# Kernel optimization log

Measured on AMD Instinct MI355X. Metric: run time of the kernel, lower is better.

The kernel has to match this reference:

```python
import jax, jax.numpy as jnp
import numpy as np
from jax import lax

N_ITER = 50  # entmax-bisect iterations (entmax library default)
DEG = 12    # neighbors per node in global item graph


def entmax_bisect(X, alpha):
    # entmax with per-row alpha, over axis=1. X: [B, L, 1], alpha: [B, 1, 1]
    d = X.shape[1]
    Xa = X * (alpha - 1.0)
    inv = 1.0 / (alpha - 1.0)
    _p = lambda z: jnp.maximum(z, 0.0) ** inv
    max_val = jnp.max(Xa, axis=1, keepdims=True)
    tau_lo = max_val - 1.0                                   # _gp(1, alpha) = 1
    tau_hi = max_val - jnp.power(1.0 / d, alpha - 1.0)       # _gp(1/d, alpha)
    f_lo = jnp.sum(_p(Xa - tau_lo), axis=1, keepdims=True) - 1.0

    def body(i, carry):
        tau_lo, dm, _ = carry
        dm = dm * 0.5
        tau_m = tau_lo + dm
        f_m = jnp.sum(_p(Xa - tau_m), axis=1, keepdims=True) - 1.0
        tau_lo = jnp.where(f_m * f_lo >= 0.0, tau_m, tau_lo)
        return (tau_lo, dm, tau_m)

    tau_lo, dm, tau_m = lax.fori_loop(0, N_ITER, body, (tau_lo, tau_hi - tau_lo, tau_lo))
    p_m = _p(Xa - tau_m)
    return p_m / jnp.sum(p_m, axis=1, keepdims=True)  # ensure_sum_one


def setup_inputs() -> dict:
    key = jax.random.key(0)
    ks = jax.random.split(key, 10)
    B, L, D, N = 1024, 50, 256, 40000
    E = N * DEG
    stdv = 1.0 / np.sqrt(D)
    u = lambda k, shape: jax.random.uniform(k, shape, jnp.float32, -stdv, stdv)

    item_emb = u(ks[0], (N, D)).at[0].set(0.0)  # padding_idx=0
    items = jax.random.randint(ks[1], (B, L), 0, N)
    inputs_seq = jax.random.randint(ks[2], (B, L), 0, N)
    alias_inputs = jax.random.randint(ks[3], (B, L), 0, L)
    target_embedding = jax.random.normal(ks[4], (B, 1, 2 * D), jnp.float32)

    # sparse global item adjacency (row-normalized, DEG neighbors per node)
    adj_rows = jnp.repeat(jnp.arange(N, dtype=jnp.int32), DEG)
    adj_cols = jax.random.randint(ks[5], (E,), 0, N, dtype=jnp.int32)
    adj_vals = jax.random.uniform(ks[6], (E,), jnp.float32) / DEG

    kp = jax.random.split(ks[7], 10)
    return {
        "items": items, "inputs_seq": inputs_seq, "alias_inputs": alias_inputs,
        "target_embedding": target_embedding, "item_emb": item_emb,
        "adj_rows": adj_rows, "adj_cols": adj_cols, "adj_vals": adj_vals,
        "wf_w": u(kp[0], (D, 2 * D)), "wf_b": u(kp[1], (D,)),
        "alphaw_w": u(kp[2], (1, D)), "alphaw_b": u(kp[3], (1,)),
        "at_w0": u(kp[4], (1, D)), "at_w1": u(kp[5], (D, D)),
        "at_w2": u(kp[6], (D, D)), "at_bias": u(kp[7], (D,)),
    }


def reference(items, inputs_seq, alias_inputs, target_embedding, item_emb,
              adj_rows, adj_cols, adj_vals, wf_w, wf_b, alphaw_w, alphaw_b,
              at_w0, at_w1, at_w2, at_bias):
    N = item_emb.shape[0]
    # GlobalItemConv (1 layer): h = (x + adj @ x) / 2 via sparse SpMM
    agg = jax.ops.segment_sum(adj_vals[:, None] * item_emb[adj_cols], adj_rows,
                              num_segments=N)
    graph_embs = (item_emb + agg) * 0.5

    hidden = graph_embs[items]                              # [B, L, D] (dropout: eval)
    target_emb = target_embedding @ wf_w.T + wf_b           # [B, 1, D]

    # get_alpha: sigmoid + 1, then masked_fill(==1 -> 1.00001)
    alpha_ent = jax.nn.sigmoid(target_emb @ alphaw_w.T + alphaw_b) + 1.0  # [B,1,1]
    alpha_ent = jnp.where(alpha_ent == 1.0, 1.00001, alpha_ent)

    # tglobal_attention
    scores = jax.nn.relu(hidden @ at_w1 + target_emb @ at_w2 + at_bias) @ at_w0.T  # [B,L,1]
    attn = entmax_bisect(scores, alpha_ent)                 # sparse softmax over L
    c = jnp.einsum('blo,bld->bod', attn, hidden)[:, 0, :]   # alpha^T @ v, squeeze -> [B,D]

    c = jax.nn.selu(c)
    return c / jnp.linalg.norm(c, axis=-1, keepdims=True)
```

## Files before the change

kernel.cpp:

```cpp
#include <hip/hip_runtime.h>
#include <hip/hip_bf16.h>
#include <math.h>

#define BB 1024
#define LL 50
#define DD 256
#define TWO_D 512
#define NN 40000
#define DEG 12
#define NITER 50

typedef __attribute__((ext_vector_type(8))) short short8;
typedef __attribute__((ext_vector_type(4))) float floatx4;

__device__ __forceinline__ float wave_sum64(float v) {
#pragma unroll
    for (int off = 32; off > 0; off >>= 1) v += __shfl_xor(v, off, 64);
    return v;
}
__device__ __forceinline__ float wave_max64(float v) {
#pragma unroll
    for (int off = 32; off > 0; off >>= 1) v = fmaxf(v, __shfl_xor(v, off, 64));
    return v;
}
__device__ __forceinline__ float bf2f(ushort u) {
    union { unsigned int i; float f; } c; c.i = ((unsigned int)u) << 16; return c.f;
}
__device__ __forceinline__ ushort f2bf(float f) {
    __hip_bfloat16 h = __float2bfloat16(f);
    return *(ushort*)&h;
}
__device__ __forceinline__ float hw_exp2(float x) { return __builtin_amdgcn_exp2f(x); }
__device__ __forceinline__ float hw_log2(float x) { return __builtin_amdgcn_logf(x); }

__global__ __launch_bounds__(256) void k_emb_bf16(
    const float* __restrict__ emb, ushort* __restrict__ ebf)
{
    int i = (blockIdx.x * 256 + threadIdx.x) * 4;
    float4 v = *(const float4*)(emb + i);
    ushort4 o;
    o.x = f2bf(v.x); o.y = f2bf(v.y); o.z = f2bf(v.z); o.w = f2bf(v.w);
    *(ushort4*)(ebf + i) = o;
}

__global__ __launch_bounds__(256) void k_conv_all_bf16(
    const ushort* __restrict__ ebf, const int* __restrict__ adj_cols,
    const float* __restrict__ adj_vals, ushort* __restrict__ gbf)
{
    int wv = threadIdx.x >> 6, lane = threadIdx.x & 63;
    int n = blockIdx.x * 4 + wv;
    int colv = 0; float valv = 0.f;
    if (lane < DEG) { colv = adj_cols[n * DEG + lane]; valv = adj_vals[n * DEG + lane]; }
    ushort4 s = *(const ushort4*)(ebf + (size_t)n * DD + lane * 4);
    float a0 = bf2f(s.x), a1 = bf2f(s.y), a2 = bf2f(s.z), a3 = bf2f(s.w);
#pragma unroll
    for (int k = 0; k < DEG; ++k) {
        int   c = __shfl(colv, k, 64);
        float v = __shfl(valv, k, 64);
        ushort4 e = *(const ushort4*)(ebf + (size_t)c * DD + lane * 4);
        a0 += v * bf2f(e.x); a1 += v * bf2f(e.y);
        a2 += v * bf2f(e.z); a3 += v * bf2f(e.w);
    }
    ushort4 o;
    o.x = f2bf(0.5f * a0); o.y = f2bf(0.5f * a1);
    o.z = f2bf(0.5f * a2); o.w = f2bf(0.5f * a3);
    *(ushort4*)(gbf + (size_t)n * DD + lane * 4) = o;
}

__global__ __launch_bounds__(256) void k_conv_all_f32(
    const float* __restrict__ emb, const int* __restrict__ adj_cols,
    const float* __restrict__ adj_vals, ushort* __restrict__ gbf)
{
    int wv = threadIdx.x >> 6, lane = threadIdx.x & 63;
    int n = blockIdx.x * 4 + wv;
    int colv = 0; float valv = 0.f;
    if (lane < DEG) { colv = adj_cols[n * DEG + lane]; valv = adj_vals[n * DEG + lane]; }
    float4 s = *(const float4*)(emb + (size_t)n * DD + lane * 4);
    float a0 = s.x, a1 = s.y, a2 = s.z, a3 = s.w;
#pragma unroll
    for (int k = 0; k < DEG; ++k) {
        int   c = __shfl(colv, k, 64);
        float v = __shfl(valv, k, 64);
        float4 e = *(const float4*)(emb + (size_t)c * DD + lane * 4);
        a0 += v * e.x; a1 += v * e.y; a2 += v * e.z; a3 += v * e.w;
    }
    ushort4 o;
    o.x = f2bf(0.5f * a0); o.y = f2bf(0.5f * a1);
    o.z = f2bf(0.5f * a2); o.w = f2bf(0.5f * a3);
    *(ushort4*)(gbf + (size_t)n * DD + lane * 4) = o;
}

__global__ __launch_bounds__(256) void k_prep_w1(
    const float* __restrict__ at_w1, ushort* __restrict__ w1t)
{
    __shared__ ushort s[4][DD];
    int k0 = blockIdx.x * 4;
    int n = threadIdx.x;
#pragma unroll
    for (int j = 0; j < 4; ++j) s[j][n] = f2bf(at_w1[(k0 + j) * DD + n]);
    __syncthreads();
    ushort4 pk;
    pk.x = s[0][n]; pk.y = s[1][n]; pk.z = s[2][n]; pk.w = s[3][n];
    *(ushort4*)(w1t + n * DD + k0) = pk;
}

__global__ __launch_bounds__(256) void k_target(
    const float* __restrict__ tgt, const float* __restrict__ wf_w,
    const float* __restrict__ wf_b, float* __restrict__ te)
{
    const int BPB = 4;
    __shared__ float x_s[BPB * TWO_D];
    int b0 = blockIdx.x * BPB;
    int tid = threadIdx.x;
    for (int i = tid; i < BPB * TWO_D; i += 256) x_s[i] = tgt[b0 * TWO_D + i];
    __syncthreads();
    float bias = wf_b[tid];
    float acc[BPB];
#pragma unroll
    for (int j = 0; j < BPB; ++j) acc[j] = bias;
    const float4* w4 = (const float4*)(wf_w + tid * TWO_D);
    for (int kk = 0; kk < TWO_D / 4; ++kk) {
        float4 w = w4[kk];
#pragma unroll
        for (int j = 0; j < BPB; ++j) {
            const float* xs = x_s + j * TWO_D + kk * 4;
            acc[j] += xs[0] * w.x + xs[1] * w.y + xs[2] * w.z + xs[3] * w.w;
        }
    }
#pragma unroll
    for (int j = 0; j < BPB; ++j) te[(b0 + j) * DD + tid] = acc[j];
}

__global__ __launch_bounds__(256) void k_t2(
    const float* __restrict__ te, const float* __restrict__ at_w2,
    const float* __restrict__ at_bias, float* __restrict__ t2)
{
    const int BPB = 4;
    __shared__ float te_s[BPB * DD];
    int b0 = blockIdx.x * BPB;
    int tid = threadIdx.x;
    for (int i = tid; i < BPB * DD; i += 256) te_s[i] = te[b0 * DD + i];
    __syncthreads();
    float bias = at_bias[tid];
    float acc[BPB];
#pragma unroll
    for (int j = 0; j < BPB; ++j) acc[j] = bias;
    for (int k = 0; k < DD; ++k) {
        float w = at_w2[k * DD + tid];
#pragma unroll
        for (int j = 0; j < BPB; ++j) acc[j] += te_s[j * DD + k] * w;
    }
#pragma unroll
    for (int j = 0; j < BPB; ++j) t2[(b0 + j) * DD + tid] = acc[j];
}

__global__ __launch_bounds__(64) void k_alpha(
    const float* __restrict__ te, const float* __restrict__ aw,
    const float* __restrict__ ab, float* __restrict__ alpha)
{
    int b = blockIdx.x;
    int lane = threadIdx.x;
    float s = 0.f;
#pragma unroll
    for (int d = 0; d < DD; d += 64) s += te[b * DD + d + lane] * aw[d + lane];
    s = wave_sum64(s);
    if (lane == 0) {
        float x = s + ab[0];
        float sig = 1.f / (1.f + expf(-x));
        float a = 1.f + sig;
        if (a == 1.f) a = 1.00001f;
        alpha[b] = a;
    }
}

__global__ __launch_bounds__(256) void k_scores_mfma(
    const int* __restrict__ items, const ushort* __restrict__ gbf,
    const ushort* __restrict__ w1t, const float* __restrict__ t2,
    const float* __restrict__ at_w0, float* __restrict__ scores)
{
    __shared__ __align__(16) ushort sA[64 * 72];
    __shared__ __align__(16) ushort sB[256 * 72];
    __shared__ float sred[64][4];
    __shared__ int s_items[64];
    int tid = threadIdx.x;
    int blk = blockIdx.x;
    int lane = tid & 63, wv = tid >> 6;
    int cn = lane & 15, q = lane >> 4;
    int n0 = wv * 64;

    if (tid < 64) s_items[tid] = items[blk * 64 + tid];
    __syncthreads();

    floatx4 acc[4][4];
#pragma unroll
    for (int mt = 0; mt < 4; ++mt)
#pragma unroll
        for (int nt = 0; nt < 4; ++nt)
            acc[mt][nt] = (floatx4){0.f, 0.f, 0.f, 0.f};

#pragma unroll 1
    for (int kc = 0; kc < 4; ++kc) {
#pragma unroll
        for (int it = 0; it < 2; ++it) {
            int i = tid + it * 256;
            int row = i >> 3, seg = i & 7;
            *(uint4*)(sA + row * 72 + seg * 8) =
                *(const uint4*)(gbf + (size_t)s_items[row] * DD + kc * 64 + seg * 8);
        }
#pragma unroll
        for (int it = 0; it < 8; ++it) {
            int i = tid + it * 256;
            int n = i >> 3, seg = i & 7;
            *(uint4*)(sB + n * 72 + seg * 8) =
                *(const uint4*)(w1t + n * DD + kc * 64 + seg * 8);
        }
        __syncthreads();
#pragma unroll
        for (int ks = 0; ks < 2; ++ks) {
            short8 af[4], bfr[4];
#pragma unroll
            for (int mt = 0; mt < 4; ++mt)
                af[mt] = *(const short8*)(sA + (mt * 16 + cn) * 72 + ks * 32 + q * 8);
#pragma unroll
            for (int nt = 0; nt < 4; ++nt)
                bfr[nt] = *(const short8*)(sB + (n0 + nt * 16 + cn) * 72 + ks * 32 + q * 8);
#pragma unroll
            for (int mt = 0; mt < 4; ++mt)
#pragma unroll
                for (int nt = 0; nt < 4; ++nt)
                    acc[mt][nt] = __builtin_amdgcn_mfma_f32_16x16x32_bf16(
                        af[mt], bfr[nt], acc[mt][nt], 0, 0, 0);
        }
        __syncthreads();
    }

    float w0v[4];
#pragma unroll
    for (int nt = 0; nt < 4; ++nt) w0v[nt] = at_w0[n0 + nt * 16 + cn];
#pragma unroll
    for (int mt = 0; mt < 4; ++mt) {
#pragma unroll
        for (int r = 0; r < 4; ++r) {
            int row_in = q * 4 + r;
            int row_g = blk * 64 + mt * 16 + row_in;
            int b = row_g / LL;
            const float* t2b = t2 + b * DD;
            float p = 0.f;
#pragma unroll
            for (int nt = 0; nt < 4; ++nt) {
                int col = n0 + nt * 16 + cn;
                float v = acc[mt][nt][r] + t2b[col];
                p += fmaxf(v, 0.f) * w0v[nt];
            }
            p += __shfl_xor(p, 1, 64);
            p += __shfl_xor(p, 2, 64);
            p += __shfl_xor(p, 4, 64);
            p += __shfl_xor(p, 8, 64);
            if (cn == 0) sred[mt * 16 + row_in][wv] = p;
        }
    }
    __syncthreads();
    if (tid < 64)
        scores[blk * 64 + tid] = sred[tid][0] + sred[tid][1] + sred[tid][2] + sred[tid][3];
}

__device__ __forceinline__ float pw(float z, float invv) {
    return hw_exp2(invv * hw_log2(z));
}

__global__ __launch_bounds__(256) void k_entmax_out(
    const float* __restrict__ scores, const float* __restrict__ alpha,
    const int* __restrict__ items, const ushort* __restrict__ gbf,
    float* __restrict__ out)
{
    __shared__ float attn_s[LL];
    __shared__ int s_it[LL];
    __shared__ float red[4];
    int b = blockIdx.x;
    int tid = threadIdx.x;

    if (tid >= 192 && tid < 192 + LL) s_it[tid - 192] = items[b * LL + (tid - 192)];

    if (tid < 64) {
        int l = tid;
        float a = alpha[b];
        float am1 = a - 1.f;
        float invv = 1.f / am1;
        float x = (l < LL) ? scores[b * LL + l] : -__builtin_inff();
        float Xa = x * am1;

        float mx = wave_max64(Xa);
        float tau_lo = mx - 1.f;
        float tau_hi = mx - hw_exp2(am1 * hw_log2(1.f / (float)LL));

        float f_lo = wave_sum64(pw(fmaxf(Xa - tau_lo, 0.f), invv)) - 1.f;

        float dm = tau_hi - tau_lo;
        float tau_m = tau_lo;
#pragma unroll 1
        for (int it = 0; it < NITER; ++it) {
            dm *= 0.5f;
            tau_m = tau_lo + dm;
            float f_m = wave_sum64(pw(fmaxf(Xa - tau_m, 0.f), invv)) - 1.f;
            if (f_m * f_lo >= 0.f) tau_lo = tau_m;
        }
        float pm = pw(fmaxf(Xa - tau_m, 0.f), invv);
        float s = wave_sum64(pm);
        if (l < LL) attn_s[l] = pm / s;
    }
    __syncthreads();

    int d = tid;
    float c = 0.f;
#pragma unroll
    for (int l = 0; l < LL; ++l)
        c += attn_s[l] * bf2f(gbf[(size_t)s_it[l] * DD + d]);

    const float SC = 1.0507009873554805f;
    const float AL = 1.6732632423543772f;
    c = SC * (c > 0.f ? c : AL * expm1f(c));

    float ss = wave_sum64(c * c);
    int wv = tid >> 6, lane = tid & 63;
    if (lane == 0) red[wv] = ss;
    __syncthreads();
    float tot = red[0] + red[1] + red[2] + red[3];
    out[b * DD + d] = c / sqrtf(tot);
}

extern "C" void kernel_launch(void* const* d_in, const int* in_sizes, int n_in,
                              void* d_out, int out_size, void* d_ws, size_t ws_size,
                              hipStream_t stream) {
    const int*   items     = (const int*)  d_in[0];
    const float* tgt       = (const float*)d_in[3];
    const float* item_emb  = (const float*)d_in[4];
    const int*   adj_cols  = (const int*)  d_in[6];
    const float* adj_vals  = (const float*)d_in[7];
    const float* wf_w      = (const float*)d_in[8];
    const float* wf_b      = (const float*)d_in[9];
    const float* alphaw_w  = (const float*)d_in[10];
    const float* alphaw_b  = (const float*)d_in[11];
    const float* at_w0     = (const float*)d_in[12];
    const float* at_w1     = (const float*)d_in[13];
    const float* at_w2     = (const float*)d_in[14];
    const float* at_bias   = (const float*)d_in[15];

    const size_t SZ_TAB = (size_t)NN * DD * sizeof(ushort);
    char* ws = (char*)d_ws;
    ushort* gbf = (ushort*)ws;   ws += SZ_TAB;
    ushort* w1t   = (ushort*)ws; ws += (size_t)DD * DD * sizeof(ushort);
    float* te     = (float*)ws;  ws += (size_t)BB * DD * sizeof(float);
    float* t2     = (float*)ws;  ws += (size_t)BB * DD * sizeof(float);
    float* alpha  = (float*)ws;  ws += ((size_t)BB + 32) * sizeof(float);
    float* scores = (float*)ws;  ws += (size_t)BB * LL * sizeof(float);
    ushort* ebf   = (ushort*)ws; ws += SZ_TAB;
    float* out    = (float*)d_out;

    size_t needA = (size_t)(ws - (char*)d_ws);
    bool pathA = ws_size >= needA;

    if (pathA) {
        k_emb_bf16<<<NN * DD / (256 * 4), 256, 0, stream>>>(item_emb, ebf);
        k_conv_all_bf16<<<NN / 4, 256, 0, stream>>>(ebf, adj_cols, adj_vals, gbf);
    } else {
        k_conv_all_f32<<<NN / 4, 256, 0, stream>>>(item_emb, adj_cols, adj_vals, gbf);
    }
    k_prep_w1<<<DD / 4, 256, 0, stream>>>(at_w1, w1t);
    k_target<<<BB / 4, 256, 0, stream>>>(tgt, wf_w, wf_b, te);
    k_t2<<<BB / 4, 256, 0, stream>>>(te, at_w2, at_bias, t2);
    k_alpha<<<BB, 64, 0, stream>>>(te, alphaw_w, alphaw_b, alpha);
    k_scores_mfma<<<(BB * LL) / 64, 256, 0, stream>>>(items, gbf, w1t, t2, at_w0, scores);
    k_entmax_out<<<BB, 256, 0, stream>>>(scores, alpha, items, gbf, out);
}
```

Measured before the change: 228.7 us.

## Precompute graph_embs @ W1 for all items and fuse scoring into entmax

Instead of gathering hidden rows per (b,l) and multiplying by W1 (51200 rows), the GEMM now runs over all 40000 table rows, writing a bf16 table G, and the scores are computed inside the entmax kernel by gathering G rows and adding t2. The three small target, t2 and alpha kernels are merged into one, and the fp32 fallback conv path is removed. This trades a slightly smaller GEMM and fewer launches for an extra 20MB table write plus gathered reads, and G is rounded to bf16 before the bias add and relu.

```diff
diff --git a/kernel.cpp b/kernel.cpp
--- a/kernel.cpp
+++ b/kernel.cpp
@@ -67,29 +67,6 @@
     *(ushort4*)(gbf + (size_t)n * DD + lane * 4) = o;
 }
 
-__global__ __launch_bounds__(256) void k_conv_all_f32(
-    const float* __restrict__ emb, const int* __restrict__ adj_cols,
-    const float* __restrict__ adj_vals, ushort* __restrict__ gbf)
-{
-    int wv = threadIdx.x >> 6, lane = threadIdx.x & 63;
-    int n = blockIdx.x * 4 + wv;
-    int colv = 0; float valv = 0.f;
-    if (lane < DEG) { colv = adj_cols[n * DEG + lane]; valv = adj_vals[n * DEG + lane]; }
-    float4 s = *(const float4*)(emb + (size_t)n * DD + lane * 4);
-    float a0 = s.x, a1 = s.y, a2 = s.z, a3 = s.w;
-#pragma unroll
-    for (int k = 0; k < DEG; ++k) {
-        int   c = __shfl(colv, k, 64);
-        float v = __shfl(valv, k, 64);
-        float4 e = *(const float4*)(emb + (size_t)c * DD + lane * 4);
-        a0 += v * e.x; a1 += v * e.y; a2 += v * e.z; a3 += v * e.w;
-    }
-    ushort4 o;
-    o.x = f2bf(0.5f * a0); o.y = f2bf(0.5f * a1);
-    o.z = f2bf(0.5f * a2); o.w = f2bf(0.5f * a3);
-    *(ushort4*)(gbf + (size_t)n * DD + lane * 4) = o;
-}
-
 __global__ __launch_bounds__(256) void k_prep_w1(
     const float* __restrict__ at_w1, ushort* __restrict__ w1t)
 {
@@ -104,92 +81,69 @@
     *(ushort4*)(w1t + n * DD + k0) = pk;
 }
 
-__global__ __launch_bounds__(256) void k_target(
+__global__ __launch_bounds__(256) void k_tprep(
     const float* __restrict__ tgt, const float* __restrict__ wf_w,
-    const float* __restrict__ wf_b, float* __restrict__ te)
-{
-    const int BPB = 4;
-    __shared__ float x_s[BPB * TWO_D];
-    int b0 = blockIdx.x * BPB;
+    const float* __restrict__ wf_b, const float* __restrict__ at_w2,
+    const float* __restrict__ at_bias, const float* __restrict__ aw,
+    const float* __restrict__ ab, float* __restrict__ t2,
+    float* __restrict__ alpha)
+{
+    __shared__ float x_s[4 * TWO_D];
+    __shared__ float te_s[4][DD];
+    int b0 = blockIdx.x * 4;
     int tid = threadIdx.x;
-    for (int i = tid; i < BPB * TWO_D; i += 256) x_s[i] = tgt[b0 * TWO_D + i];
-    __syncthreads();
+    int wv = tid >> 6, lane = tid & 63;
+    for (int i = tid; i < 4 * TWO_D; i += 256) x_s[i] = tgt[b0 * TWO_D + i];
+    __syncthreads();
+
     float bias = wf_b[tid];
-    float acc[BPB];
-#pragma unroll
-    for (int j = 0; j < BPB; ++j) acc[j] = bias;
+    float acc[4] = {bias, bias, bias, bias};
     const float4* w4 = (const float4*)(wf_w + tid * TWO_D);
     for (int kk = 0; kk < TWO_D / 4; ++kk) {
         float4 w = w4[kk];
 #pragma unroll
-        for (int j = 0; j < BPB; ++j) {
+        for (int j = 0; j < 4; ++j) {
             const float* xs = x_s + j * TWO_D + kk * 4;
             acc[j] += xs[0] * w.x + xs[1] * w.y + xs[2] * w.z + xs[3] * w.w;
         }
     }
 #pragma unroll
-    for (int j = 0; j < BPB; ++j) te[(b0 + j) * DD + tid] = acc[j];
-}
-
-__global__ __launch_bounds__(256) void k_t2(
-    const float* __restrict__ te, const float* __restrict__ at_w2,
-    const float* __restrict__ at_bias, float* __restrict__ t2)
-{
-    const int BPB = 4;
-    __shared__ float te_s[BPB * DD];
-    int b0 = blockIdx.x * BPB;
-    int tid = threadIdx.x;
-    for (int i = tid; i < BPB * DD; i += 256) te_s[i] = te[b0 * DD + i];
-    __syncthreads();
-    float bias = at_bias[tid];
-    float acc[BPB];
-#pragma unroll
-    for (int j = 0; j < BPB; ++j) acc[j] = bias;
+    for (int j = 0; j < 4; ++j) te_s[j][tid] = acc[j];
+    __syncthreads();
+
+    float bias2 = at_bias[tid];
+    float acc2[4] = {bias2, bias2, bias2, bias2};
     for (int k = 0; k < DD; ++k) {
         float w = at_w2[k * DD + tid];
 #pragma unroll
-        for (int j = 0; j < BPB; ++j) acc[j] += te_s[j * DD + k] * w;
-    }
-#pragma unroll
-    for (int j = 0; j < BPB; ++j) t2[(b0 + j) * DD + tid] = acc[j];
-}
-
-__global__ __launch_bounds__(64) void k_alpha(
-    const float* __restrict__ te, const float* __restrict__ aw,
-    const float* __restrict__ ab, float* __restrict__ alpha)
-{
-    int b = blockIdx.x;
-    int lane = threadIdx.x;
-    float s = 0.f;
-#pragma unroll
-    for (int d = 0; d < DD; d += 64) s += te[b * DD + d + lane] * aw[d + lane];
+        for (int j = 0; j < 4; ++j) acc2[j] += te_s[j][k] * w;
+    }
+#pragma unroll
+    for (int j = 0; j < 4; ++j) t2[(b0 + j) * DD + tid] = acc2[j];
+
+    float s = te_s[wv][lane] * aw[lane] + te_s[wv][lane + 64] * aw[lane + 64]
+            + te_s[wv][lane + 128] * aw[lane + 128] + te_s[wv][lane + 192] * aw[lane + 192];
     s = wave_sum64(s);
     if (lane == 0) {
         float x = s + ab[0];
-        float sig = 1.f / (1.f + expf(-x));
-        float a = 1.f + sig;
+        float a = 1.f + 1.f / (1.f + expf(-x));
         if (a == 1.f) a = 1.00001f;
-        alpha[b] = a;
-    }
-}
-
-__global__ __launch_bounds__(256) void k_scores_mfma(
-    const int* __restrict__ items, const ushort* __restrict__ gbf,
-    const ushort* __restrict__ w1t, const float* __restrict__ t2,
-    const float* __restrict__ at_w0, float* __restrict__ scores)
+        alpha[b0 + wv] = a;
+    }
+}
+
+__global__ __launch_bounds__(256) void k_gw1(
+    const ushort* __restrict__ gbf, const ushort* __restrict__ w1t,
+    ushort* __restrict__ G)
 {
     __shared__ __align__(16) ushort sA[64 * 72];
     __shared__ __align__(16) ushort sB[256 * 72];
-    __shared__ float sred[64][4];
-    __shared__ int s_items[64];
     int tid = threadIdx.x;
     int blk = blockIdx.x;
     int lane = tid & 63, wv = tid >> 6;
     int cn = lane & 15, q = lane >> 4;
     int n0 = wv * 64;
-
-    if (tid < 64) s_items[tid] = items[blk * 64 + tid];
-    __syncthreads();
+    const size_t rowbase = (size_t)blk * 64;
 
     floatx4 acc[4][4];
 #pragma unroll
@@ -205,7 +159,7 @@
             int i = tid + it * 256;
             int row = i >> 3, seg = i & 7;
             *(uint4*)(sA + row * 72 + seg * 8) =
-                *(const uint4*)(gbf + (size_t)s_items[row] * DD + kc * 64 + seg * 8);
+                *(const uint4*)(gbf + (rowbase + row) * DD + kc * 64 + seg * 8);
         }
 #pragma unroll
         for (int it = 0; it < 8; ++it) {
@@ -234,59 +188,62 @@
         __syncthreads();
     }
 
-    float w0v[4];
-#pragma unroll
-    for (int nt = 0; nt < 4; ++nt) w0v[nt] = at_w0[n0 + nt * 16 + cn];
-#pragma unroll
-    for (int mt = 0; mt < 4; ++mt) {
-#pragma unroll
-        for (int r = 0; r < 4; ++r) {
-            int row_in = q * 4 + r;
-            int row_g = blk * 64 + mt * 16 + row_in;
-            int b = row_g / LL;
-            const float* t2b = t2 + b * DD;
-            float p = 0.f;
-#pragma unroll
-            for (int nt = 0; nt < 4; ++nt) {
-                int col = n0 + nt * 16 + cn;
-                float v = acc[mt][nt][r] + t2b[col];
-                p += fmaxf(v, 0.f) * w0v[nt];
-            }
-            p += __shfl_xor(p, 1, 64);
-            p += __shfl_xor(p, 2, 64);
-            p += __shfl_xor(p, 4, 64);
-            p += __shfl_xor(p, 8, 64);
-            if (cn == 0) sred[mt * 16 + row_in][wv] = p;
-        }
-    }
-    __syncthreads();
-    if (tid < 64)
-        scores[blk * 64 + tid] = sred[tid][0] + sred[tid][1] + sred[tid][2] + sred[tid][3];
+    ushort (*oS)[DD] = (ushort(*)[DD])sB;
+#pragma unroll
+    for (int mt = 0; mt < 4; ++mt)
+#pragma unroll
+        for (int nt = 0; nt < 4; ++nt)
+#pragma unroll
+            for (int r = 0; r < 4; ++r)
+                oS[mt * 16 + q * 4 + r][n0 + nt * 16 + cn] = f2bf(acc[mt][nt][r]);
+    __syncthreads();
+#pragma unroll
+    for (int it = 0; it < 8; ++it) {
+        int i = tid + it * 256;
+        int row = i >> 5, seg = i & 31;
+        *(uint4*)(G + (rowbase + row) * DD + seg * 8) = *(const uint4*)(&oS[row][seg * 8]);
+    }
 }
 
 __device__ __forceinline__ float pw(float z, float invv) {
     return hw_exp2(invv * hw_log2(z));
 }
 
-__global__ __launch_bounds__(256) void k_entmax_out(
-    const float* __restrict__ scores, const float* __restrict__ alpha,
-    const int* __restrict__ items, const ushort* __restrict__ gbf,
+__global__ __launch_bounds__(256) void k_fused_entmax(
+    const int* __restrict__ items, const ushort* __restrict__ G,
+    const ushort* __restrict__ gbf, const float* __restrict__ t2,
+    const float* __restrict__ alpha, const float* __restrict__ at_w0,
     float* __restrict__ out)
 {
+    __shared__ int s_it[LL];
+    __shared__ float sred[LL][4];
     __shared__ float attn_s[LL];
-    __shared__ int s_it[LL];
     __shared__ float red[4];
     int b = blockIdx.x;
     int tid = threadIdx.x;
-
-    if (tid >= 192 && tid < 192 + LL) s_it[tid - 192] = items[b * LL + (tid - 192)];
+    int lane = tid & 63, wv = tid >> 6;
+
+    if (tid < LL) s_it[tid] = items[b * LL + tid];
+    __syncthreads();
+
+    float t2v = t2[b * DD + tid];
+    float w0v = at_w0[tid];
+#pragma unroll
+    for (int l = 0; l < LL; ++l) {
+        float g = bf2f(G[(size_t)s_it[l] * DD + tid]);
+        float p = fmaxf(g + t2v, 0.f) * w0v;
+        p = wave_sum64(p);
+        if (lane == 0) sred[l][wv] = p;
+    }
+    __syncthreads();
 
     if (tid < 64) {
         int l = tid;
+        float x = (l < LL) ? (sred[l][0] + sred[l][1] + sred[l][2] + sred[l][3])
+                           : -__builtin_inff();
         float a = alpha[b];
         float am1 = a - 1.f;
         float invv = 1.f / am1;
-        float x = (l < LL) ? scores[b * LL + l] : -__builtin_inff();
         float Xa = x * am1;
 
         float mx = wave_max64(Xa);
@@ -310,22 +267,20 @@
     }
     __syncthreads();
 
-    int d = tid;
     float c = 0.f;
 #pragma unroll
     for (int l = 0; l < LL; ++l)
-        c += attn_s[l] * bf2f(gbf[(size_t)s_it[l] * DD + d]);
+        c += attn_s[l] * bf2f(gbf[(size_t)s_it[l] * DD + tid]);
 
     const float SC = 1.0507009873554805f;
     const float AL = 1.6732632423543772f;
     c = SC * (c > 0.f ? c : AL * expm1f(c));
 
     float ss = wave_sum64(c * c);
-    int wv = tid >> 6, lane = tid & 63;
     if (lane == 0) red[wv] = ss;
     __syncthreads();
     float tot = red[0] + red[1] + red[2] + red[3];
-    out[b * DD + d] = c / sqrtf(tot);
+    out[b * DD + tid] = c / sqrtf(tot);
 }
 
 extern "C" void kernel_launch(void* const* d_in, const int* in_sizes, int n_in,
@@ -348,27 +303,18 @@
     const size_t SZ_TAB = (size_t)NN * DD * sizeof(ushort);
     char* ws = (char*)d_ws;
     ushort* gbf = (ushort*)ws;   ws += SZ_TAB;
-    ushort* w1t   = (ushort*)ws; ws += (size_t)DD * DD * sizeof(ushort);
-    float* te     = (float*)ws;  ws += (size_t)BB * DD * sizeof(float);
-    float* t2     = (float*)ws;  ws += (size_t)BB * DD * sizeof(float);
-    float* alpha  = (float*)ws;  ws += ((size_t)BB + 32) * sizeof(float);
-    float* scores = (float*)ws;  ws += (size_t)BB * LL * sizeof(float);
-    ushort* ebf   = (ushort*)ws; ws += SZ_TAB;
-    float* out    = (float*)d_out;
-
-    size_t needA = (size_t)(ws - (char*)d_ws);
-    bool pathA = ws_size >= needA;
-
-    if (pathA) {
-        k_emb_bf16<<<NN * DD / (256 * 4), 256, 0, stream>>>(item_emb, ebf);
-        k_conv_all_bf16<<<NN / 4, 256, 0, stream>>>(ebf, adj_cols, adj_vals, gbf);
-    } else {
-        k_conv_all_f32<<<NN / 4, 256, 0, stream>>>(item_emb, adj_cols, adj_vals, gbf);
-    }
+    ushort* Gbf = (ushort*)ws;   ws += SZ_TAB;
+    ushort* ebf = (ushort*)ws;   ws += SZ_TAB;
+    ushort* w1t = (ushort*)ws;   ws += (size_t)DD * DD * sizeof(ushort);
+    float* t2    = (float*)ws;   ws += (size_t)BB * DD * sizeof(float);
+    float* alpha = (float*)ws;   ws += ((size_t)BB + 32) * sizeof(float);
+    float* out   = (float*)d_out;
+
+    k_emb_bf16<<<NN * DD / (256 * 4), 256, 0, stream>>>(item_emb, ebf);
+    k_conv_all_bf16<<<NN / 4, 256, 0, stream>>>(ebf, adj_cols, adj_vals, gbf);
     k_prep_w1<<<DD / 4, 256, 0, stream>>>(at_w1, w1t);
-    k_target<<<BB / 4, 256, 0, stream>>>(tgt, wf_w, wf_b, te);
-    k_t2<<<BB / 4, 256, 0, stream>>>(te, at_w2, at_bias, t2);
-    k_alpha<<<BB, 64, 0, stream>>>(te, alphaw_w, alphaw_b, alpha);
-    k_scores_mfma<<<(BB * LL) / 64, 256, 0, stream>>>(items, gbf, w1t, t2, at_w0, scores);
-    k_entmax_out<<<BB, 256, 0, stream>>>(scores, alpha, items, gbf, out);
-}
+    k_tprep<<<BB / 4, 256, 0, stream>>>(tgt, wf_w, wf_b, at_w2, at_bias,
+                                        alphaw_w, alphaw_b, t2, alpha);
+    k_gw1<<<NN / 64, 256, 0, stream>>>(gbf, w1t, Gbf);
+    k_fused_entmax<<<BB, 256, 0, stream>>>(items, Gbf, gbf, t2, alpha, at_w0, out);
+}
```

Measured after the change: 244.6 us. 1.07x slower.

## Merge independent prep kernels into two block-partitioned launches and batch gathers

Applied to the files above, without the earlier changes.

Independent preprocessing kernels are combined into two launches that pick their role by block index. The first converts embeddings to bf16, transposes W1 and computes the target projection. The second runs the graph conv together with the t2 projection and alpha. This cuts the launch count from about eight to four and lets small kernels overlap with the large streaming ones. The conv loop now issues all 12 neighbor loads before accumulating, for more memory-level parallelism at the cost of extra registers, and the f32 fallback path for a small workspace is dropped.

```diff
diff --git a/kernel.cpp b/kernel.cpp
--- a/kernel.cpp
+++ b/kernel.cpp
@@ -33,143 +33,113 @@
 __device__ __forceinline__ float hw_exp2(float x) { return __builtin_amdgcn_exp2f(x); }
 __device__ __forceinline__ float hw_log2(float x) { return __builtin_amdgcn_logf(x); }
 
-__global__ __launch_bounds__(256) void k_emb_bf16(
-    const float* __restrict__ emb, ushort* __restrict__ ebf)
-{
-    int i = (blockIdx.x * 256 + threadIdx.x) * 4;
-    float4 v = *(const float4*)(emb + i);
-    ushort4 o;
-    o.x = f2bf(v.x); o.y = f2bf(v.y); o.z = f2bf(v.z); o.w = f2bf(v.w);
-    *(ushort4*)(ebf + i) = o;
-}
-
-__global__ __launch_bounds__(256) void k_conv_all_bf16(
-    const ushort* __restrict__ ebf, const int* __restrict__ adj_cols,
-    const float* __restrict__ adj_vals, ushort* __restrict__ gbf)
-{
-    int wv = threadIdx.x >> 6, lane = threadIdx.x & 63;
-    int n = blockIdx.x * 4 + wv;
-    int colv = 0; float valv = 0.f;
-    if (lane < DEG) { colv = adj_cols[n * DEG + lane]; valv = adj_vals[n * DEG + lane]; }
-    ushort4 s = *(const ushort4*)(ebf + (size_t)n * DD + lane * 4);
-    float a0 = bf2f(s.x), a1 = bf2f(s.y), a2 = bf2f(s.z), a3 = bf2f(s.w);
-#pragma unroll
-    for (int k = 0; k < DEG; ++k) {
-        int   c = __shfl(colv, k, 64);
-        float v = __shfl(valv, k, 64);
-        ushort4 e = *(const ushort4*)(ebf + (size_t)c * DD + lane * 4);
-        a0 += v * bf2f(e.x); a1 += v * bf2f(e.y);
-        a2 += v * bf2f(e.z); a3 += v * bf2f(e.w);
-    }
-    ushort4 o;
-    o.x = f2bf(0.5f * a0); o.y = f2bf(0.5f * a1);
-    o.z = f2bf(0.5f * a2); o.w = f2bf(0.5f * a3);
-    *(ushort4*)(gbf + (size_t)n * DD + lane * 4) = o;
-}
-
-__global__ __launch_bounds__(256) void k_conv_all_f32(
-    const float* __restrict__ emb, const int* __restrict__ adj_cols,
-    const float* __restrict__ adj_vals, ushort* __restrict__ gbf)
-{
-    int wv = threadIdx.x >> 6, lane = threadIdx.x & 63;
-    int n = blockIdx.x * 4 + wv;
-    int colv = 0; float valv = 0.f;
-    if (lane < DEG) { colv = adj_cols[n * DEG + lane]; valv = adj_vals[n * DEG + lane]; }
-    float4 s = *(const float4*)(emb + (size_t)n * DD + lane * 4);
-    float a0 = s.x, a1 = s.y, a2 = s.z, a3 = s.w;
-#pragma unroll
-    for (int k = 0; k < DEG; ++k) {
-        int   c = __shfl(colv, k, 64);
-        float v = __shfl(valv, k, 64);
-        float4 e = *(const float4*)(emb + (size_t)c * DD + lane * 4);
-        a0 += v * e.x; a1 += v * e.y; a2 += v * e.z; a3 += v * e.w;
-    }
-    ushort4 o;
-    o.x = f2bf(0.5f * a0); o.y = f2bf(0.5f * a1);
-    o.z = f2bf(0.5f * a2); o.w = f2bf(0.5f * a3);
-    *(ushort4*)(gbf + (size_t)n * DD + lane * 4) = o;
-}
-
-__global__ __launch_bounds__(256) void k_prep_w1(
-    const float* __restrict__ at_w1, ushort* __restrict__ w1t)
-{
-    __shared__ ushort s[4][DD];
-    int k0 = blockIdx.x * 4;
-    int n = threadIdx.x;
-#pragma unroll
-    for (int j = 0; j < 4; ++j) s[j][n] = f2bf(at_w1[(k0 + j) * DD + n]);
-    __syncthreads();
-    ushort4 pk;
-    pk.x = s[0][n]; pk.y = s[1][n]; pk.z = s[2][n]; pk.w = s[3][n];
-    *(ushort4*)(w1t + n * DD + k0) = pk;
-}
-
-__global__ __launch_bounds__(256) void k_target(
+__global__ __launch_bounds__(256) void k_mega1(
+    const float* __restrict__ emb, ushort* __restrict__ ebf,
+    const float* __restrict__ at_w1, ushort* __restrict__ w1t,
     const float* __restrict__ tgt, const float* __restrict__ wf_w,
     const float* __restrict__ wf_b, float* __restrict__ te)
 {
-    const int BPB = 4;
-    __shared__ float x_s[BPB * TWO_D];
-    int b0 = blockIdx.x * BPB;
+    __shared__ __align__(16) char smem[8192];
+    int bid = blockIdx.x;
     int tid = threadIdx.x;
-    for (int i = tid; i < BPB * TWO_D; i += 256) x_s[i] = tgt[b0 * TWO_D + i];
-    __syncthreads();
-    float bias = wf_b[tid];
-    float acc[BPB];
-#pragma unroll
-    for (int j = 0; j < BPB; ++j) acc[j] = bias;
-    const float4* w4 = (const float4*)(wf_w + tid * TWO_D);
-    for (int kk = 0; kk < TWO_D / 4; ++kk) {
-        float4 w = w4[kk];
-#pragma unroll
-        for (int j = 0; j < BPB; ++j) {
-            const float* xs = x_s + j * TWO_D + kk * 4;
-            acc[j] += xs[0] * w.x + xs[1] * w.y + xs[2] * w.z + xs[3] * w.w;
-        }
-    }
-#pragma unroll
-    for (int j = 0; j < BPB; ++j) te[(b0 + j) * DD + tid] = acc[j];
-}
-
-__global__ __launch_bounds__(256) void k_t2(
+
+    if (bid < 10000) {
+        int i = (bid * 256 + tid) * 4;
+        float4 v = *(const float4*)(emb + i);
+        ushort4 o;
+        o.x = f2bf(v.x); o.y = f2bf(v.y); o.z = f2bf(v.z); o.w = f2bf(v.w);
+        *(ushort4*)(ebf + i) = o;
+    } else if (bid < 10064) {
+        ushort (*s)[DD] = (ushort(*)[DD])smem;
+        int k0 = (bid - 10000) * 4;
+#pragma unroll
+        for (int j = 0; j < 4; ++j) s[j][tid] = f2bf(at_w1[(k0 + j) * DD + tid]);
+        __syncthreads();
+        ushort4 pk;
+        pk.x = s[0][tid]; pk.y = s[1][tid]; pk.z = s[2][tid]; pk.w = s[3][tid];
+        *(ushort4*)(w1t + tid * DD + k0) = pk;
+    } else {
+        float* x_s = (float*)smem;
+        int b0 = (bid - 10064) * 4;
+        for (int i = tid; i < 4 * TWO_D; i += 256) x_s[i] = tgt[b0 * TWO_D + i];
+        __syncthreads();
+        float bias = wf_b[tid];
+        float acc[4] = {bias, bias, bias, bias};
+        const float4* w4 = (const float4*)(wf_w + tid * TWO_D);
+        for (int kk = 0; kk < TWO_D / 4; ++kk) {
+            float4 w = w4[kk];
+#pragma unroll
+            for (int j = 0; j < 4; ++j) {
+                const float* xs = x_s + j * TWO_D + kk * 4;
+                acc[j] += xs[0] * w.x + xs[1] * w.y + xs[2] * w.z + xs[3] * w.w;
+            }
+        }
+#pragma unroll
+        for (int j = 0; j < 4; ++j) te[(b0 + j) * DD + tid] = acc[j];
+    }
+}
+
+__global__ __launch_bounds__(256) void k_mega2(
+    const ushort* __restrict__ ebf, const int* __restrict__ adj_cols,
+    const float* __restrict__ adj_vals, ushort* __restrict__ gbf,
     const float* __restrict__ te, const float* __restrict__ at_w2,
-    const float* __restrict__ at_bias, float* __restrict__ t2)
+    const float* __restrict__ at_bias, const float* __restrict__ aw,
+    const float* __restrict__ ab, float* __restrict__ t2,
+    float* __restrict__ alpha)
 {
-    const int BPB = 4;
-    __shared__ float te_s[BPB * DD];
-    int b0 = blockIdx.x * BPB;
+    __shared__ float te_s[4][DD];
+    int bid = blockIdx.x;
     int tid = threadIdx.x;
-    for (int i = tid; i < BPB * DD; i += 256) te_s[i] = te[b0 * DD + i];
-    __syncthreads();
-    float bias = at_bias[tid];
-    float acc[BPB];
-#pragma unroll
-    for (int j = 0; j < BPB; ++j) acc[j] = bias;
-    for (int k = 0; k < DD; ++k) {
-        float w = at_w2[k * DD + tid];
-#pragma unroll
-        for (int j = 0; j < BPB; ++j) acc[j] += te_s[j * DD + k] * w;
-    }
-#pragma unroll
-    for (int j = 0; j < BPB; ++j) t2[(b0 + j) * DD + tid] = acc[j];
-}
-
-__global__ __launch_bounds__(64) void k_alpha(
-    const float* __restrict__ te, const float* __restrict__ aw,
-    const float* __restrict__ ab, float* __restrict__ alpha)
-{
-    int b = blockIdx.x;
-    int lane = threadIdx.x;
-    float s = 0.f;
-#pragma unroll
-    for (int d = 0; d < DD; d += 64) s += te[b * DD + d + lane] * aw[d + lane];
-    s = wave_sum64(s);
-    if (lane == 0) {
-        float x = s + ab[0];
-        float sig = 1.f / (1.f + expf(-x));
-        float a = 1.f + sig;
-        if (a == 1.f) a = 1.00001f;
-        alpha[b] = a;
+    int wv = tid >> 6, lane = tid & 63;
+
+    if (bid < 10000) {
+        int n = bid * 4 + wv;
+        int colv = 0; float valv = 0.f;
+        if (lane < DEG) { colv = adj_cols[n * DEG + lane]; valv = adj_vals[n * DEG + lane]; }
+        int cols[DEG]; float vals[DEG];
+#pragma unroll
+        for (int k = 0; k < DEG; ++k) {
+            cols[k] = __shfl(colv, k, 64);
+            vals[k] = __shfl(valv, k, 64);
+        }
+        ushort4 s = *(const ushort4*)(ebf + (size_t)n * DD + lane * 4);
+        ushort4 e[DEG];
+#pragma unroll
+        for (int k = 0; k < DEG; ++k)
+            e[k] = *(const ushort4*)(ebf + (size_t)cols[k] * DD + lane * 4);
+        float a0 = bf2f(s.x), a1 = bf2f(s.y), a2 = bf2f(s.z), a3 = bf2f(s.w);
+#pragma unroll
+        for (int k = 0; k < DEG; ++k) {
+            float v = vals[k];
+            a0 += v * bf2f(e[k].x); a1 += v * bf2f(e[k].y);
+            a2 += v * bf2f(e[k].z); a3 += v * bf2f(e[k].w);
+        }
+        ushort4 o;
+        o.x = f2bf(0.5f * a0); o.y = f2bf(0.5f * a1);
+        o.z = f2bf(0.5f * a2); o.w = f2bf(0.5f * a3);
+        *(ushort4*)(gbf + (size_t)n * DD + lane * 4) = o;
+    } else {
+        int b0 = (bid - 10000) * 4;
+        for (int i = tid; i < 4 * DD; i += 256) te_s[i >> 8][i & 255] = te[b0 * DD + i];
+        __syncthreads();
+        float bias2 = at_bias[tid];
+        float acc2[4] = {bias2, bias2, bias2, bias2};
+        for (int k = 0; k < DD; ++k) {
+            float w = at_w2[k * DD + tid];
+#pragma unroll
+            for (int j = 0; j < 4; ++j) acc2[j] += te_s[j][k] * w;
+        }
+#pragma unroll
+        for (int j = 0; j < 4; ++j) t2[(b0 + j) * DD + tid] = acc2[j];
+
+        float s = te_s[wv][lane] * aw[lane] + te_s[wv][lane + 64] * aw[lane + 64]
+                + te_s[wv][lane + 128] * aw[lane + 128] + te_s[wv][lane + 192] * aw[lane + 192];
+        s = wave_sum64(s);
+        if (lane == 0) {
+            float a = 1.f + 1.f / (1.f + expf(-(s + ab[0])));
+            if (a == 1.f) a = 1.00001f;
+            alpha[b0 + wv] = a;
+        }
     }
 }
 
@@ -348,27 +318,19 @@
     const size_t SZ_TAB = (size_t)NN * DD * sizeof(ushort);
     char* ws = (char*)d_ws;
     ushort* gbf = (ushort*)ws;   ws += SZ_TAB;
-    ushort* w1t   = (ushort*)ws; ws += (size_t)DD * DD * sizeof(ushort);
+    ushort* ebf = (ushort*)ws;   ws += SZ_TAB;
+    ushort* w1t = (ushort*)ws;   ws += (size_t)DD * DD * sizeof(ushort);
     float* te     = (float*)ws;  ws += (size_t)BB * DD * sizeof(float);
     float* t2     = (float*)ws;  ws += (size_t)BB * DD * sizeof(float);
     float* alpha  = (float*)ws;  ws += ((size_t)BB + 32) * sizeof(float);
     float* scores = (float*)ws;  ws += (size_t)BB * LL * sizeof(float);
-    ushort* ebf   = (ushort*)ws; ws += SZ_TAB;
     float* out    = (float*)d_out;
 
-    size_t needA = (size_t)(ws - (char*)d_ws);
-    bool pathA = ws_size >= needA;
-
-    if (pathA) {
-        k_emb_bf16<<<NN * DD / (256 * 4), 256, 0, stream>>>(item_emb, ebf);
-        k_conv_all_bf16<<<NN / 4, 256, 0, stream>>>(ebf, adj_cols, adj_vals, gbf);
-    } else {
-        k_conv_all_f32<<<NN / 4, 256, 0, stream>>>(item_emb, adj_cols, adj_vals, gbf);
-    }
-    k_prep_w1<<<DD / 4, 256, 0, stream>>>(at_w1, w1t);
-    k_target<<<BB / 4, 256, 0, stream>>>(tgt, wf_w, wf_b, te);
-    k_t2<<<BB / 4, 256, 0, stream>>>(te, at_w2, at_bias, t2);
-    k_alpha<<<BB, 64, 0, stream>>>(te, alphaw_w, alphaw_b, alpha);
+    k_mega1<<<10320, 256, 0, stream>>>(item_emb, ebf, at_w1, w1t,
+                                       tgt, wf_w, wf_b, te);
+    k_mega2<<<10256, 256, 0, stream>>>(ebf, adj_cols, adj_vals, gbf,
+                                       te, at_w2, at_bias,
+                                       alphaw_w, alphaw_b, t2, alpha);
     k_scores_mfma<<<(BB * LL) / 64, 256, 0, stream>>>(items, gbf, w1t, t2, at_w0, scores);
     k_entmax_out<<<BB, 256, 0, stream>>>(scores, alpha, items, gbf, out);
 }
```

New measurement: 273.0 us. +19.4%, slower.
